# Optimization experiments

Measured on AMD Instinct MI355X. Metric: run time of the kernel, lower is better.

The kernel has to match this reference:

```python
import jax, jax.numpy as jnp
import numpy as np

B, L, C, H = 8, 1024, 384, 6
D = C // H          # head_dim = 64
K, N = 2, 4         # radial_degree, angular_degree
EPS = 1e-5


def setup_inputs() -> dict:
    key = jax.random.key(0)
    ks = jax.random.split(key, 8)
    x = jax.random.normal(ks[0], (B, L, C), dtype=jnp.float32)
    pos = jax.random.uniform(ks[1], (B, L, 2), dtype=jnp.float32) * 32.0
    w_norm = jnp.ones((C,), dtype=jnp.float32)
    w_in = jax.random.normal(ks[2], (3 * C, C), dtype=jnp.float32) * 0.02
    b_in = jnp.zeros((3 * C,), dtype=jnp.float32)
    w_out = jax.random.normal(ks[3], (C, C), dtype=jnp.float32) * 0.02
    b_out = jnp.zeros((C,), dtype=jnp.float32)
    b_coef = jax.random.normal(ks[4], (H, K + 1, N + 1), dtype=jnp.float32) * 0.01
    b_coef = b_coef.at[:, 1, 0].set(1.0)  # reset_parameters fills b[..., 1, 0] = 1
    c_coef = jax.random.normal(ks[5], (H, K + 1, N + 1), dtype=jnp.float32) * 0.01
    return {"x": x, "pos": pos, "w_norm": w_norm, "w_in": w_in, "b_in": b_in,
            "w_out": w_out, "b_out": b_out, "b_coef": b_coef, "c_coef": c_coef}


def _polar_bias(pos, b_coef, c_coef):
    # pos: (B, L, 2) -> bias grid (B, H, L, L)
    dist = pos[:, :, None, :] - pos[:, None, :, :]           # (B, Lq, Lk, 2)
    theta = jnp.arctan2(dist[..., 1], dist[..., 0])          # (B, Lq, Lk)
    r = jnp.sqrt(jnp.sum(dist * dist, axis=-1))              # (B, Lq, Lk)
    r_pow = r[..., None] ** jnp.arange(K + 1, dtype=r.dtype)           # (B, Lq, Lk, K+1)
    ang = theta[..., None] * jnp.arange(N + 1, dtype=theta.dtype)      # (B, Lq, Lk, N+1)
    cos_part = jnp.einsum('hkn,bijk,bijn->bhij', b_coef, r_pow, jnp.cos(ang))
    sin_part = jnp.einsum('hkn,bijk,bijn->bhij', c_coef, r_pow, jnp.sin(ang))
    return cos_part + sin_part


def reference(x, pos, w_norm, w_in, b_in, w_out, b_out, b_coef, c_coef):
    # RMSNorm
    ms = jnp.mean(x * x, axis=-1, keepdims=True)
    xn = x * jax.lax.rsqrt(ms + EPS) * w_norm
    # packed QKV projection
    qkv = xn @ w_in.T + b_in                                  # (B, L, 3C)
    q, k, v = jnp.split(qkv, 3, axis=-1)
    def heads(t):  # (B, L, C) -> (B, H, L, D)
        return t.reshape(B, L, H, D).transpose(0, 2, 1, 3)
    q, k, v = heads(q), heads(k), heads(v)
    bias = _polar_bias(pos, b_coef, c_coef)                   # (B, H, L, L)
    scores = jnp.einsum('bhqd,bhkd->bhqk', q, k) / jnp.sqrt(jnp.float32(D)) + bias
    attn = jax.nn.softmax(scores, axis=-1)
    o = jnp.einsum('bhqk,bhkd->bhqd', attn, v)                # (B, H, L, D)
    o = o.transpose(0, 2, 1, 3).reshape(B, L, C)
    return o @ w_out.T + b_out
```

## Files before the change

### kernel.cpp

```cpp
#include <hip/hip_runtime.h>

typedef unsigned int  u32;
typedef unsigned short u16;
typedef __attribute__((ext_vector_type(8))) short short8;
typedef __attribute__((ext_vector_type(4))) float f32x4;

__device__ __forceinline__ u16 f2bf(float x) {
  union { float f; u32 u; } un; un.f = x;
  u32 r = un.u + 0x7FFFu + ((un.u >> 16) & 1u);
  return (u16)(r >> 16);
}
__device__ __forceinline__ f32x4 mfma_bf16(short8 a, short8 b, f32x4 c) {
  return __builtin_amdgcn_mfma_f32_16x16x32_bf16(a, b, c, 0, 0, 0);
}

__global__ __launch_bounds__(256) void prep_kernel(
    const float* __restrict__ x, const float* __restrict__ w_norm,
    const float* __restrict__ w_in, const float* __restrict__ w_out,
    u16* __restrict__ xn, u16* __restrict__ winb, u16* __restrict__ woutb)
{
  int blk = blockIdx.x, t = threadIdx.x;
  if (blk < 2048) {
    int wv = t >> 6, lane = t & 63;
    int row = blk * 4 + wv;
    const float* xr = x + (size_t)row * 384;
    float v[6]; float ss = 0.f;
    #pragma unroll
    for (int i = 0; i < 6; i++) { v[i] = xr[lane + 64 * i]; ss += v[i] * v[i]; }
    #pragma unroll
    for (int off = 32; off > 0; off >>= 1) ss += __shfl_xor(ss, off);
    float rs = __builtin_amdgcn_rsqf(ss * (1.0f / 384.0f) + 1e-5f);
    #pragma unroll
    for (int i = 0; i < 6; i++) {
      float xv = v[i] * rs * w_norm[lane + 64 * i];
      xn[(size_t)row * 384 + lane + 64 * i] = f2bf(xv);
    }
  } else {
    int base = (blk - 2048) * 2048 + t * 8;
    #pragma unroll
    for (int j = 0; j < 8; j++) {
      int idx = base + j;
      if (idx < 442368) winb[idx] = f2bf(w_in[idx]);
      else              woutb[idx - 442368] = f2bf(w_out[idx - 442368]);
    }
  }
}

template<bool OUT_F32, bool QSCALE>
__global__ __launch_bounds__(256) void gemm_kernel(
    const u16* __restrict__ A, int lda,
    const u16* __restrict__ Bw, int ldb,
    const float* __restrict__ bias, void* __restrict__ outp, int ldc, int K)
{
  __shared__ __attribute__((aligned(16))) u16 As[128 * 72];
  __shared__ __attribute__((aligned(16))) u16 Bs[128 * 72];
  int t = threadIdx.x;
  int lane = t & 63, wv = t >> 6;
  int g = lane >> 4, cl = lane & 15;
  int row0 = blockIdx.x * 128, col0 = blockIdx.y * 128;
  int wm = (wv >> 1) * 64, wn = (wv & 1) * 64;
  f32x4 acc[4][4];
  #pragma unroll
  for (int i = 0; i < 4; i++)
    #pragma unroll
    for (int j = 0; j < 4; j++) acc[i][j] = (f32x4){0.f, 0.f, 0.f, 0.f};

  for (int k0 = 0; k0 < K; k0 += 64) {
    __syncthreads();
    #pragma unroll
    for (int j = 0; j < 4; j++) {
      int i = t + 256 * j;
      int r = i >> 3, ch = i & 7;
      *(uint4*)(&As[r * 72 + ch * 8]) =
          *(const uint4*)(A + (size_t)(row0 + r) * lda + k0 + ch * 8);
      *(uint4*)(&Bs[r * 72 + ch * 8]) =
          *(const uint4*)(Bw + (size_t)(col0 + r) * ldb + k0 + ch * 8);
    }
    __syncthreads();
    #pragma unroll
    for (int kh = 0; kh < 2; kh++) {
      short8 af[4], bfr[4];
      #pragma unroll
      for (int s = 0; s < 4; s++) {
        af[s]  = *(const short8*)(&As[(wm + s * 16 + cl) * 72 + kh * 32 + g * 8]);
        bfr[s] = *(const short8*)(&Bs[(wn + s * 16 + cl) * 72 + kh * 32 + g * 8]);
      }
      #pragma unroll
      for (int i = 0; i < 4; i++)
        #pragma unroll
        for (int j = 0; j < 4; j++)
          acc[i][j] = mfma_bf16(af[i], bfr[j], acc[i][j]);
    }
  }
  #pragma unroll
  for (int i = 0; i < 4; i++) {
    #pragma unroll
    for (int j = 0; j < 4; j++) {
      int colb = col0 + wn + j * 16 + cl;
      float bv = bias[colb];
      #pragma unroll
      for (int r = 0; r < 4; r++) {
        int rowb = row0 + wm + i * 16 + g * 4 + r;
        float v = acc[i][j][r] + bv;
        if (QSCALE) { if (colb < 384) v *= 0.125f; }
        if (OUT_F32) ((float*)outp)[(size_t)rowb * ldc + colb] = v;
        else ((u16*)outp)[(size_t)rowb * ldc + colb] = f2bf(v);
      }
    }
  }
}

__global__ __launch_bounds__(512) void attn_hybrid4(
    const u16* __restrict__ qkv, const float* __restrict__ pos,
    const float* __restrict__ bcf, const float* __restrict__ ccf,
    u16* __restrict__ obuf)
{
  __shared__ __attribute__((aligned(16))) float sbuf[2][64][66];
  __shared__ __attribute__((aligned(16))) u16 vsmem[2][64][72];
  __shared__ float mlbuf[2][4][16];

  int bid = blockIdx.x;
  int xslot = bid & 7, rest = bid >> 3;
  int qt = rest & 15, gdiv = rest >> 4;
  int g48 = gdiv * 8 + xslot;
  int b = g48 / 6, h = g48 - b * 6;

  int t = threadIdx.x, lane = t & 63, wv = t >> 6;
  int strip = wv & 3, half = wv >> 2;
  int g = lane >> 4, cl = lane & 15;

  float bc[15], cc[15];
  #pragma unroll
  for (int i = 0; i < 15; i++) { bc[i] = bcf[h * 15 + i]; cc[i] = ccf[h * 15 + i]; }

  const u16* qbase =
      qkv + (size_t)(b * 1024 + qt * 64 + strip * 16 + cl) * 1152 + h * 64;
  short8 qf0 = *(const short8*)(qbase + g * 8);
  short8 qf1 = *(const short8*)(qbase + 32 + g * 8);

  float qx[4], qy[4];
  #pragma unroll
  for (int r = 0; r < 4; r++) {
    int qr = qt * 64 + strip * 16 + 4 * g + r;
    qx[r] = pos[(size_t)(b * 1024 + qr) * 2 + 0];
    qy[r] = pos[(size_t)(b * 1024 + qr) * 2 + 1];
  }

  f32x4 oa[4];
  #pragma unroll
  for (int d = 0; d < 4; d++) oa[d] = (f32x4){0.f, 0.f, 0.f, 0.f};
  float m_own = -1e30f, l_own = 0.f;

  const u16* kb = qkv + (size_t)b * 1024 * 1152 + 384 + h * 64;
  const u16* vsrc = qkv + (size_t)b * 1024 * 1152 + 768 + h * 64 + strip * 16;
  const float* pb = pos + (size_t)b * 2048;

  for (int kt = 0; kt < 512; kt += 64) {
    int k0 = half * 512 + kt;
    {
      const u16* vr = vsrc + (size_t)(k0 + lane) * 1152;
      uint4 w0 = *(const uint4*)(vr);
      uint4 w1 = *(const uint4*)(vr + 8);
      int vd = strip * 16;
      vsmem[half][vd + 0][lane] = (u16)(w0.x);  vsmem[half][vd + 1][lane] = (u16)(w0.x >> 16);
      vsmem[half][vd + 2][lane] = (u16)(w0.y);  vsmem[half][vd + 3][lane] = (u16)(w0.y >> 16);
      vsmem[half][vd + 4][lane] = (u16)(w0.z);  vsmem[half][vd + 5][lane] = (u16)(w0.z >> 16);
      vsmem[half][vd + 6][lane] = (u16)(w0.w);  vsmem[half][vd + 7][lane] = (u16)(w0.w >> 16);
      vsmem[half][vd + 8][lane] = (u16)(w1.x);  vsmem[half][vd + 9][lane] = (u16)(w1.x >> 16);
      vsmem[half][vd +10][lane] = (u16)(w1.y);  vsmem[half][vd +11][lane] = (u16)(w1.y >> 16);
      vsmem[half][vd +12][lane] = (u16)(w1.z);  vsmem[half][vd +13][lane] = (u16)(w1.z >> 16);
      vsmem[half][vd +14][lane] = (u16)(w1.w);  vsmem[half][vd +15][lane] = (u16)(w1.w >> 16);
    }
    f32x4 s[4];
    #pragma unroll
    for (int ks = 0; ks < 4; ks++) {
      const u16* kr = kb + (size_t)(k0 + ks * 16 + cl) * 1152;
      short8 kf0 = *(const short8*)(kr + g * 8);
      short8 kf1 = *(const short8*)(kr + 32 + g * 8);
      f32x4 z = (f32x4){0.f, 0.f, 0.f, 0.f};
      z = mfma_bf16(qf0, kf0, z);
      z = mfma_bf16(qf1, kf1, z);
      s[ks] = z;
    }
    #pragma unroll
    for (int ks = 0; ks < 4; ks++) {
      int kidx = k0 + ks * 16 + cl;
      float kx = pb[kidx * 2], ky = pb[kidx * 2 + 1];
      #pragma unroll
      for (int r = 0; r < 4; r++) {
        float dx = qx[r] - kx, dy = qy[r] - ky;
        float r2 = dx * dx + dy * dy;
        bool zz = !(r2 > 0.f);
        float ir = zz ? 0.f : __builtin_amdgcn_rsqf(r2);
        float rr = r2 * ir;
        float c1 = zz ? 1.f : dx * ir;
        float s1 = dy * ir;
        float c2 = c1*c1 - s1*s1, s2 = 2.f*c1*s1;
        float c3 = c1*c2 - s1*s2, s3 = s1*c2 + c1*s2;
        float c4 = c2*c2 - s2*s2, s4 = 2.f*c2*s2;
        float a0 = bc[0] + bc[1]*c1 + bc[2]*c2 + bc[3]*c3 + bc[4]*c4
                 + cc[1]*s1 + cc[2]*s2 + cc[3]*s3 + cc[4]*s4;
        float a1 = bc[5] + bc[6]*c1 + bc[7]*c2 + bc[8]*c3 + bc[9]*c4
                 + cc[6]*s1 + cc[7]*s2 + cc[8]*s3 + cc[9]*s4;
        float a2 = bc[10] + bc[11]*c1 + bc[12]*c2 + bc[13]*c3 + bc[14]*c4
                 + cc[11]*s1 + cc[12]*s2 + cc[13]*s3 + cc[14]*s4;
        sbuf[half][strip * 16 + 4 * g + r][ks * 16 + cl] =
            s[ks][r] + a0 + rr * (a1 + rr * a2);
      }
    }
    __syncthreads();
    {
      int rown = strip * 16 + cl, cb = g * 16;
      float tmax = -1e30f;
      #pragma unroll
      for (int c = 0; c < 16; c++) tmax = fmaxf(tmax, sbuf[half][rown][cb + c]);
      tmax = fmaxf(tmax, __shfl_xor(tmax, 16));
      tmax = fmaxf(tmax, __shfl_xor(tmax, 32));
      float mn = fmaxf(m_own, tmax);
      float sc = __builtin_amdgcn_exp2f((m_own - mn) * 1.44269504f);
      m_own = mn;
      #pragma unroll
      for (int r = 0; r < 4; r++) {
        float scr = __shfl(sc, 4 * g + r);
        #pragma unroll
        for (int d = 0; d < 4; d++) oa[d][r] *= scr;
      }
      float psum = 0.f;
      union { u16 u[8]; short8 s8; } pk0, pk1;
      const float* srow = &sbuf[half][strip * 16 + cl][0];
      #pragma unroll
      for (int j = 0; j < 8; j++) {
        float p = __builtin_amdgcn_exp2f((srow[8 * g + j] - mn) * 1.44269504f);
        psum += p; pk0.u[j] = f2bf(p);
      }
      #pragma unroll
      for (int j = 0; j < 8; j++) {
        float p = __builtin_amdgcn_exp2f((srow[32 + 8 * g + j] - mn) * 1.44269504f);
        psum += p; pk1.u[j] = f2bf(p);
      }
      psum += __shfl_xor(psum, 16);
      psum += __shfl_xor(psum, 32);
      l_own = l_own * sc + psum;
      #pragma unroll
      for (int d = 0; d < 4; d++) {
        short8 vf0 = *(const short8*)(&vsmem[half][d * 16 + cl][g * 8]);
        short8 vf1 = *(const short8*)(&vsmem[half][d * 16 + cl][32 + g * 8]);
        oa[d] = mfma_bf16(pk0.s8, vf0, oa[d]);
        oa[d] = mfma_bf16(pk1.s8, vf1, oa[d]);
      }
    }
    __syncthreads();
  }
  float* o1 = &sbuf[0][0][0];
  if (half == 1) {
    if (lane < 16) { mlbuf[0][strip][lane] = m_own; mlbuf[1][strip][lane] = l_own; }
    #pragma unroll
    for (int r = 0; r < 4; r++) {
      int row = 4 * g + r;
      #pragma unroll
      for (int d = 0; d < 4; d++)
        o1[(strip * 16 + row) * 64 + d * 16 + cl] = oa[d][r];
    }
  }
  __syncthreads();
  if (half == 0) {
    float m1 = mlbuf[0][strip][cl], l1 = mlbuf[1][strip][cl];
    float M  = fmaxf(m_own, m1);
    float f0 = __builtin_amdgcn_exp2f((m_own - M) * 1.44269504f);
    float f1 = __builtin_amdgcn_exp2f((m1    - M) * 1.44269504f);
    float linv = __builtin_amdgcn_rcpf(l_own * f0 + l1 * f1);
    #pragma unroll
    for (int r = 0; r < 4; r++) {
      int row = 4 * g + r;
      float f0r = __shfl(f0, row), f1r = __shfl(f1, row), invr = __shfl(linv, row);
      int qr = qt * 64 + strip * 16 + row;
      #pragma unroll
      for (int d = 0; d < 4; d++) {
        float val = (oa[d][r] * f0r +
                     o1[(strip * 16 + row) * 64 + d * 16 + cl] * f1r) * invr;
        obuf[(size_t)(b * 1024 + qr) * 384 + h * 64 + d * 16 + cl] = f2bf(val);
      }
    }
  }
}

extern "C" void kernel_launch(void* const* d_in, const int* in_sizes, int n_in,
                              void* d_out, int out_size, void* d_ws, size_t ws_size,
                              hipStream_t stream) {
  const float* x      = (const float*)d_in[0];
  const float* pos    = (const float*)d_in[1];
  const float* w_norm = (const float*)d_in[2];
  const float* w_in   = (const float*)d_in[3];
  const float* b_in   = (const float*)d_in[4];
  const float* w_out  = (const float*)d_in[5];
  const float* b_out  = (const float*)d_in[6];
  const float* b_coef = (const float*)d_in[7];
  const float* c_coef = (const float*)d_in[8];

  char* ws = (char*)d_ws;
  u16* xn    = (u16*)(ws + 0);
  u16* obuf  = (u16*)(ws + 0);
  u16* winb  = (u16*)(ws + 6291456);
  u16* woutb = (u16*)(ws + 7176192);
  u16* qkvb  = (u16*)(ws + 7471104);

  prep_kernel<<<2336, 256, 0, stream>>>(x, w_norm, w_in, w_out, xn, winb, woutb);
  gemm_kernel<false, true><<<dim3(64, 9), 256, 0, stream>>>(
      xn, 384, winb, 384, b_in, qkvb, 1152, 384);
  attn_hybrid4<<<768, 512, 0, stream>>>(qkvb, pos, b_coef, c_coef, obuf);
  gemm_kernel<true, false><<<dim3(64, 3), 256, 0, stream>>>(
      obuf, 384, woutb, 384, b_out, (float*)d_out, 384, 384);
}
```

Measured before the change: 167.1 us.

## Swap QK MFMA operands to keep softmax in registers and drop score LDS

```diff
diff --git a/kernel.cpp b/kernel.cpp
--- a/kernel.cpp
+++ b/kernel.cpp
@@ -9,6 +9,11 @@
   union { float f; u32 u; } un; un.f = x;
   u32 r = un.u + 0x7FFFu + ((un.u >> 16) & 1u);
   return (u16)(r >> 16);
+}
+__device__ __forceinline__ u32 cvtpk(float lo, float hi) {
+  u32 r;
+  asm("v_cvt_pk_bf16_f32 %0, %1, %2" : "=v"(r) : "v"(lo), "v"(hi));
+  return r;
 }
 __device__ __forceinline__ f32x4 mfma_bf16(short8 a, short8 b, f32x4 c) {
   return __builtin_amdgcn_mfma_f32_16x16x32_bf16(a, b, c, 0, 0, 0);
@@ -110,66 +115,66 @@
   }
 }
 
-__global__ __launch_bounds__(512) void attn_hybrid4(
+__global__ __launch_bounds__(256) void attn_swap(
     const u16* __restrict__ qkv, const float* __restrict__ pos,
     const float* __restrict__ bcf, const float* __restrict__ ccf,
     u16* __restrict__ obuf)
 {
-  __shared__ __attribute__((aligned(16))) float sbuf[2][64][66];
   __shared__ __attribute__((aligned(16))) u16 vsmem[2][64][72];
-  __shared__ float mlbuf[2][4][16];
+  __shared__ float mlbuf[2][2][16];
 
   int bid = blockIdx.x;
   int xslot = bid & 7, rest = bid >> 3;
-  int qt = rest & 15, gdiv = rest >> 4;
+  int qt = rest & 31, gdiv = rest >> 5;
   int g48 = gdiv * 8 + xslot;
   int b = g48 / 6, h = g48 - b * 6;
 
   int t = threadIdx.x, lane = t & 63, wv = t >> 6;
-  int strip = wv & 3, half = wv >> 2;
+  int strip = wv & 1, half = wv >> 1;
   int g = lane >> 4, cl = lane & 15;
 
   float bc[15], cc[15];
   #pragma unroll
   for (int i = 0; i < 15; i++) { bc[i] = bcf[h * 15 + i]; cc[i] = ccf[h * 15 + i]; }
 
-  const u16* qbase =
-      qkv + (size_t)(b * 1024 + qt * 64 + strip * 16 + cl) * 1152 + h * 64;
+  int qrow = qt * 32 + strip * 16 + cl;
+  const u16* qbase = qkv + (size_t)(b * 1024 + qrow) * 1152 + h * 64;
   short8 qf0 = *(const short8*)(qbase + g * 8);
   short8 qf1 = *(const short8*)(qbase + 32 + g * 8);
-
-  float qx[4], qy[4];
-  #pragma unroll
-  for (int r = 0; r < 4; r++) {
-    int qr = qt * 64 + strip * 16 + 4 * g + r;
-    qx[r] = pos[(size_t)(b * 1024 + qr) * 2 + 0];
-    qy[r] = pos[(size_t)(b * 1024 + qr) * 2 + 1];
-  }
+  float qx = pos[(size_t)(b * 1024 + qrow) * 2 + 0];
+  float qy = pos[(size_t)(b * 1024 + qrow) * 2 + 1];
 
   f32x4 oa[4];
   #pragma unroll
   for (int d = 0; d < 4; d++) oa[d] = (f32x4){0.f, 0.f, 0.f, 0.f};
   float m_own = -1e30f, l_own = 0.f;
 
-  const u16* kb = qkv + (size_t)b * 1024 * 1152 + 384 + h * 64;
-  const u16* vsrc = qkv + (size_t)b * 1024 * 1152 + 768 + h * 64 + strip * 16;
+  const u16* kb   = qkv + (size_t)b * 1024 * 1152 + 384 + h * 64;
+  const u16* vsrc = qkv + (size_t)b * 1024 * 1152 + 768 + h * 64 + strip * 32;
   const float* pb = pos + (size_t)b * 2048;
+
+  int phys = (lane & 0x23) | ((lane & 0x0C) << 1) | ((lane & 0x10) >> 2);
+  u16* vcol = &vsmem[half][0][0] + phys;
 
   for (int kt = 0; kt < 512; kt += 64) {
     int k0 = half * 512 + kt;
     {
       const u16* vr = vsrc + (size_t)(k0 + lane) * 1152;
-      uint4 w0 = *(const uint4*)(vr);
-      uint4 w1 = *(const uint4*)(vr + 8);
-      int vd = strip * 16;
-      vsmem[half][vd + 0][lane] = (u16)(w0.x);  vsmem[half][vd + 1][lane] = (u16)(w0.x >> 16);
-      vsmem[half][vd + 2][lane] = (u16)(w0.y);  vsmem[half][vd + 3][lane] = (u16)(w0.y >> 16);
-      vsmem[half][vd + 4][lane] = (u16)(w0.z);  vsmem[half][vd + 5][lane] = (u16)(w0.z >> 16);
-      vsmem[half][vd + 6][lane] = (u16)(w0.w);  vsmem[half][vd + 7][lane] = (u16)(w0.w >> 16);
-      vsmem[half][vd + 8][lane] = (u16)(w1.x);  vsmem[half][vd + 9][lane] = (u16)(w1.x >> 16);
-      vsmem[half][vd +10][lane] = (u16)(w1.y);  vsmem[half][vd +11][lane] = (u16)(w1.y >> 16);
-      vsmem[half][vd +12][lane] = (u16)(w1.z);  vsmem[half][vd +13][lane] = (u16)(w1.z >> 16);
-      vsmem[half][vd +14][lane] = (u16)(w1.w);  vsmem[half][vd +15][lane] = (u16)(w1.w >> 16);
+      uint4 a0 = *(const uint4*)(vr);
+      uint4 a1 = *(const uint4*)(vr + 8);
+      uint4 a2 = *(const uint4*)(vr + 16);
+      uint4 a3 = *(const uint4*)(vr + 24);
+      u16* c0 = vcol + (size_t)(strip * 32) * 72;
+      #define ST(i, val) c0[(size_t)(i) * 72] = (u16)(val)
+      ST(0,  a0.x); ST(1,  a0.x >> 16); ST(2,  a0.y); ST(3,  a0.y >> 16);
+      ST(4,  a0.z); ST(5,  a0.z >> 16); ST(6,  a0.w); ST(7,  a0.w >> 16);
+      ST(8,  a1.x); ST(9,  a1.x >> 16); ST(10, a1.y); ST(11, a1.y >> 16);
+      ST(12, a1.z); ST(13, a1.z >> 16); ST(14, a1.w); ST(15, a1.w >> 16);
+      ST(16, a2.x); ST(17, a2.x >> 16); ST(18, a2.y); ST(19, a2.y >> 16);
+      ST(20, a2.z); ST(21, a2.z >> 16); ST(22, a2.w); ST(23, a2.w >> 16);
+      ST(24, a3.x); ST(25, a3.x >> 16); ST(26, a3.y); ST(27, a3.y >> 16);
+      ST(28, a3.z); ST(29, a3.z >> 16); ST(30, a3.w); ST(31, a3.w >> 16);
+      #undef ST
     }
     f32x4 s[4];
     #pragma unroll
@@ -178,17 +183,20 @@
       short8 kf0 = *(const short8*)(kr + g * 8);
       short8 kf1 = *(const short8*)(kr + 32 + g * 8);
       f32x4 z = (f32x4){0.f, 0.f, 0.f, 0.f};
-      z = mfma_bf16(qf0, kf0, z);
-      z = mfma_bf16(qf1, kf1, z);
+      z = mfma_bf16(kf0, qf0, z);
+      z = mfma_bf16(kf1, qf1, z);
       s[ks] = z;
     }
     #pragma unroll
     for (int ks = 0; ks < 4; ks++) {
-      int kidx = k0 + ks * 16 + cl;
-      float kx = pb[kidx * 2], ky = pb[kidx * 2 + 1];
+      int kbase4 = k0 + ks * 16 + 4 * g;
+      float4 pA = *(const float4*)(pb + (size_t)kbase4 * 2);
+      float4 pB = *(const float4*)(pb + (size_t)kbase4 * 2 + 4);
+      float kxs[4] = {pA.x, pA.z, pB.x, pB.z};
+      float kys[4] = {pA.y, pA.w, pB.y, pB.w};
       #pragma unroll
       for (int r = 0; r < 4; r++) {
-        float dx = qx[r] - kx, dy = qy[r] - ky;
+        float dx = qx - kxs[r], dy = qy - kys[r];
         float r2 = dx * dx + dy * dy;
         bool zz = !(r2 > 0.f);
         float ir = zz ? 0.f : __builtin_amdgcn_rsqf(r2);
@@ -204,54 +212,52 @@
                  + cc[6]*s1 + cc[7]*s2 + cc[8]*s3 + cc[9]*s4;
         float a2 = bc[10] + bc[11]*c1 + bc[12]*c2 + bc[13]*c3 + bc[14]*c4
                  + cc[11]*s1 + cc[12]*s2 + cc[13]*s3 + cc[14]*s4;
-        sbuf[half][strip * 16 + 4 * g + r][ks * 16 + cl] =
-            s[ks][r] + a0 + rr * (a1 + rr * a2);
-      }
-    }
+        s[ks][r] += a0 + rr * (a1 + rr * a2);
+      }
+    }
+    float tmax = -1e30f;
+    #pragma unroll
+    for (int ks = 0; ks < 4; ks++)
+      #pragma unroll
+      for (int r = 0; r < 4; r++) tmax = fmaxf(tmax, s[ks][r]);
+    tmax = fmaxf(tmax, __shfl_xor(tmax, 16));
+    tmax = fmaxf(tmax, __shfl_xor(tmax, 32));
+    float mn = fmaxf(m_own, tmax);
+    float sc = __builtin_amdgcn_exp2f((m_own - mn) * 1.44269504f);
+    m_own = mn;
+    #pragma unroll
+    for (int r = 0; r < 4; r++) {
+      float scr = __shfl(sc, 4 * g + r);
+      #pragma unroll
+      for (int d = 0; d < 4; d++) oa[d][r] *= scr;
+    }
+    float psum = 0.f;
+    #pragma unroll
+    for (int ks = 0; ks < 4; ks++)
+      #pragma unroll
+      for (int r = 0; r < 4; r++) {
+        float p = __builtin_amdgcn_exp2f((s[ks][r] - mn) * 1.44269504f);
+        psum += p; s[ks][r] = p;
+      }
+    psum += __shfl_xor(psum, 16);
+    psum += __shfl_xor(psum, 32);
+    l_own = l_own * sc + psum;
+    union { u32 w[4]; short8 s8; } pk0, pk1;
+    pk0.w[0] = cvtpk(s[0][0], s[0][1]); pk0.w[1] = cvtpk(s[0][2], s[0][3]);
+    pk0.w[2] = cvtpk(s[1][0], s[1][1]); pk0.w[3] = cvtpk(s[1][2], s[1][3]);
+    pk1.w[0] = cvtpk(s[2][0], s[2][1]); pk1.w[1] = cvtpk(s[2][2], s[2][3]);
+    pk1.w[2] = cvtpk(s[3][0], s[3][1]); pk1.w[3] = cvtpk(s[3][2], s[3][3]);
     __syncthreads();
-    {
-      int rown = strip * 16 + cl, cb = g * 16;
-      float tmax = -1e30f;
-      #pragma unroll
-      for (int c = 0; c < 16; c++) tmax = fmaxf(tmax, sbuf[half][rown][cb + c]);
-      tmax = fmaxf(tmax, __shfl_xor(tmax, 16));
-      tmax = fmaxf(tmax, __shfl_xor(tmax, 32));
-      float mn = fmaxf(m_own, tmax);
-      float sc = __builtin_amdgcn_exp2f((m_own - mn) * 1.44269504f);
-      m_own = mn;
-      #pragma unroll
-      for (int r = 0; r < 4; r++) {
-        float scr = __shfl(sc, 4 * g + r);
-        #pragma unroll
-        for (int d = 0; d < 4; d++) oa[d][r] *= scr;
-      }
-      float psum = 0.f;
-      union { u16 u[8]; short8 s8; } pk0, pk1;
-      const float* srow = &sbuf[half][strip * 16 + cl][0];
-      #pragma unroll
-      for (int j = 0; j < 8; j++) {
-        float p = __builtin_amdgcn_exp2f((srow[8 * g + j] - mn) * 1.44269504f);
-        psum += p; pk0.u[j] = f2bf(p);
-      }
-      #pragma unroll
-      for (int j = 0; j < 8; j++) {
-        float p = __builtin_amdgcn_exp2f((srow[32 + 8 * g + j] - mn) * 1.44269504f);
-        psum += p; pk1.u[j] = f2bf(p);
-      }
-      psum += __shfl_xor(psum, 16);
-      psum += __shfl_xor(psum, 32);
-      l_own = l_own * sc + psum;
-      #pragma unroll
-      for (int d = 0; d < 4; d++) {
-        short8 vf0 = *(const short8*)(&vsmem[half][d * 16 + cl][g * 8]);
-        short8 vf1 = *(const short8*)(&vsmem[half][d * 16 + cl][32 + g * 8]);
-        oa[d] = mfma_bf16(pk0.s8, vf0, oa[d]);
-        oa[d] = mfma_bf16(pk1.s8, vf1, oa[d]);
-      }
+    #pragma unroll
+    for (int d = 0; d < 4; d++) {
+      short8 vf0 = *(const short8*)(&vsmem[half][d * 16 + cl][g * 8]);
+      short8 vf1 = *(const short8*)(&vsmem[half][d * 16 + cl][32 + g * 8]);
+      oa[d] = mfma_bf16(pk0.s8, vf0, oa[d]);
+      oa[d] = mfma_bf16(pk1.s8, vf1, oa[d]);
     }
     __syncthreads();
   }
-  float* o1 = &sbuf[0][0][0];
+  float* o1 = (float*)&vsmem[0][0][0];
   if (half == 1) {
     if (lane < 16) { mlbuf[0][strip][lane] = m_own; mlbuf[1][strip][lane] = l_own; }
     #pragma unroll
@@ -273,7 +279,7 @@
     for (int r = 0; r < 4; r++) {
       int row = 4 * g + r;
       float f0r = __shfl(f0, row), f1r = __shfl(f1, row), invr = __shfl(linv, row);
-      int qr = qt * 64 + strip * 16 + row;
+      int qr = qt * 32 + strip * 16 + row;
       #pragma unroll
       for (int d = 0; d < 4; d++) {
         float val = (oa[d][r] * f0r +
@@ -307,7 +313,7 @@
   prep_kernel<<<2336, 256, 0, stream>>>(x, w_norm, w_in, w_out, xn, winb, woutb);
   gemm_kernel<false, true><<<dim3(64, 9), 256, 0, stream>>>(
       xn, 384, winb, 384, b_in, qkvb, 1152, 384);
-  attn_hybrid4<<<768, 512, 0, stream>>>(qkvb, pos, b_coef, c_coef, obuf);
+  attn_swap<<<1536, 256, 0, stream>>>(qkvb, pos, b_coef, c_coef, obuf);
   gemm_kernel<true, false><<<dim3(64, 3), 256, 0, stream>>>(
       obuf, 384, woutb, 384, b_out, (float*)d_out, 384, 384);
 }
```

Measured after the change: 168.0 us. No clear change (+0.5%).
